# Optimization experiments

Measured on AMD Instinct MI355X. Metric: run time of the kernel, lower is better.

The kernel has to match this reference:

```python
import jax, jax.numpy as jnp
import numpy as np

N_NODES = 50000
N_EDGES = 600000
D_IN = 128
D_HID = 128


def _graph_conv(x, src, dst, W, b, n_nodes):
    # DGL GraphConv with norm='both': out = D_in^{-1/2} A (D_out^{-1/2} x) W + b
    ones = jnp.ones(src.shape[0], dtype=x.dtype)
    deg_out = jnp.maximum(jax.ops.segment_sum(ones, src, num_segments=n_nodes), 1.0)
    deg_in = jnp.maximum(jax.ops.segment_sum(ones, dst, num_segments=n_nodes), 1.0)
    h = x * (deg_out ** -0.5)[:, None]            # [N, d] scale by src-side norm
    agg = jax.ops.segment_sum(h[src], dst, num_segments=n_nodes)  # SpMM aggregate
    agg = agg * (deg_in ** -0.5)[:, None]
    return agg @ W + b


def _two_layer(x, src, dst, W1, b1, W2, b2):
    h = jax.nn.relu(_graph_conv(x, src, dst, W1, b1, N_NODES))
    return jax.nn.relu(_graph_conv(h, src, dst, W2, b2, N_NODES))


def setup_inputs() -> dict:
    key = jax.random.key(0)
    ks = jax.random.split(key, 16)
    inp = {}
    for i in range(4):
        inp[f"x{i+1}"] = jax.random.normal(ks[3 * i], (N_NODES, D_IN), dtype=jnp.float32)
        inp[f"src{i+1}"] = jax.random.randint(ks[3 * i + 1], (N_EDGES,), 0, N_NODES)
        inp[f"dst{i+1}"] = jax.random.randint(ks[3 * i + 2], (N_EDGES,), 0, N_NODES)
    inp["W1"] = jax.random.normal(ks[12], (D_IN, D_HID), dtype=jnp.float32) * (D_IN ** -0.5)
    inp["b1"] = jnp.zeros((D_HID,), dtype=jnp.float32)
    inp["W2"] = jax.random.normal(ks[13], (D_HID, D_HID), dtype=jnp.float32) * (D_HID ** -0.5)
    inp["b2"] = jnp.zeros((D_HID,), dtype=jnp.float32)
    return inp


def reference(x1, src1, dst1, x2, src2, dst2, x3, src3, dst3, x4, src4, dst4,
              W1, b1, W2, b2):
    h1 = _two_layer(x1, src1, dst1, W1, b1, W2, b2)
    h2 = _two_layer(x2, src2, dst2, W1, b1, W2, b2)
    h3 = _two_layer(x3, src3, dst3, W1, b1, W2, b2)
    h4 = _two_layer(x4, src4, dst4, W1, b1, W2, b2)
    # multi_graph_opt='mean': concat along node axis, mean over nodes -> [D_HID]
    x = jnp.mean(jnp.concatenate([h1, h2, h3, h4], axis=0), axis=0)
    # output_opt='mean': scalar
    return jnp.mean(x)
```

## Files before the change

kernel.cpp:

```cpp
#include <hip/hip_runtime.h>
#include <hip/hip_bf16.h>

#define N_NODES 50000
#define N_EDGES 600000
#define D 128

#define NBUCK 64
#define BUCK_R 782
#define BCAP 16384
#define EPB 2048

typedef __attribute__((ext_vector_type(8))) short bf16x8;
typedef __attribute__((ext_vector_type(4))) float f32x4;
typedef __attribute__((ext_vector_type(2))) float f32x2;

__device__ __forceinline__ const int* pick4(const int* a, const int* b,
                                            const int* c, const int* d, int g) {
    return g == 0 ? a : g == 1 ? b : g == 2 ? c : d;
}
__device__ __forceinline__ const float4* pick4f(const float4* a, const float4* b,
                                                const float4* c, const float4* d, int g) {
    return g == 0 ? a : g == 1 ? b : g == 2 ? c : d;
}

__device__ __forceinline__ unsigned bfpair(float a, float b) {
    unsigned ua = __float_as_uint(a); ua = (ua + 0x7FFF + ((ua >> 16) & 1)) >> 16;
    unsigned ub = __float_as_uint(b); ub = (ub + 0x7FFF + ((ub >> 16) & 1)) >> 16;
    return ua | (ub << 16);
}

__global__ __launch_bounds__(256) void phaseA_kernel(
        const int* s0, const int* s1, const int* s2, const int* s3,
        const int* d0, const int* d1, const int* d2, const int* d3,
        int* __restrict__ bCurD, int* __restrict__ bCurS,
        int* __restrict__ pairs, unsigned short* __restrict__ svals, int nEdges) {
    int gi = blockIdx.y;
    const int* src = pick4(s0, s1, s2, s3, gi);
    const int* dst = pick4(d0, d1, d2, d3, gi);
    int* pg = pairs + (size_t)gi * NBUCK * BCAP;
    unsigned short* sg = svals + (size_t)gi * NBUCK * BCAP;

    __shared__ int cntD[64], cntS[64], gposD[64], gposS[64], lcurD[64], lcurS[64];
    int t = threadIdx.x;
    if (t < 64) { cntD[t] = 0; cntS[t] = 0; }
    __syncthreads();

    int myD[8], myS[8];
    int base = blockIdx.x * EPB + t;
    #pragma unroll
    for (int j = 0; j < 8; ++j) {
        int e = base + j * 256;
        if (e < nEdges) {
            myD[j] = dst[e]; myS[j] = src[e];
            atomicAdd(&cntD[myD[j] / BUCK_R], 1);
            atomicAdd(&cntS[myS[j] / BUCK_R], 1);
        } else myD[j] = -1;
    }
    __syncthreads();
    if (t < 64) {
        int c = cntD[t];
        gposD[t] = t * BCAP + (c ? atomicAdd(&bCurD[gi * 64 + t], c) : 0);
        lcurD[t] = 0;
        c = cntS[t];
        gposS[t] = t * BCAP + (c ? atomicAdd(&bCurS[gi * 64 + t], c) : 0);
        lcurS[t] = 0;
    }
    __syncthreads();
    #pragma unroll
    for (int j = 0; j < 8; ++j) {
        if (myD[j] >= 0) {
            int bD = myD[j] / BUCK_R, bS = myS[j] / BUCK_R;
            int lp = atomicAdd(&lcurD[bD], 1);
            pg[gposD[bD] + lp] = ((myD[j] - bD * BUCK_R) << 16) | myS[j];
            int ls = atomicAdd(&lcurS[bS], 1);
            sg[gposS[bS] + ls] = (unsigned short)(myS[j] - bS * BUCK_R);
        }
    }
}

__global__ __launch_bounds__(256) void csrB_kernel(
        const int* __restrict__ bCurD, const int* __restrict__ pairs,
        int* __restrict__ rowptrBase, int* __restrict__ eixBase,
        float* __restrict__ rsIBase) {
    int gi = blockIdx.y, b = blockIdx.x;
    int* rowptr = rowptrBase + (size_t)gi * (N_NODES + 1);
    int* eidx = eixBase + (size_t)gi * N_EDGES;
    float* rsI = rsIBase + (size_t)gi * N_NODES;
    const int* pg = pairs + ((size_t)gi * NBUCK + b) * BCAP;
    const int* bCur = bCurD + gi * 64;

    __shared__ int P[BCAP];
    __shared__ int cnt[1024];
    __shared__ int cur[1024];
    __shared__ int wpart[4];
    __shared__ int sbase;

    int t = threadIdx.x;
    int nb = bCur[b]; if (nb > BCAP) nb = BCAP;

    if (t < 64) {
        int v = (t < b) ? min(bCur[t], BCAP) : 0;
        for (int off = 32; off; off >>= 1) v += __shfl_down(v, off, 64);
        if (t == 0) sbase = v;
    }
    for (int i = t; i < 1024; i += 256) cnt[i] = 0;
    __syncthreads();
    int base = sbase;

    for (int i = t; i < nb; i += 256) {
        int p = pg[i];
        P[i] = p;
        atomicAdd(&cnt[p >> 16], 1);
    }
    __syncthreads();

    int c0 = cnt[t * 4 + 0], c1 = cnt[t * 4 + 1], c2 = cnt[t * 4 + 2], c3 = cnt[t * 4 + 3];
    int ts = c0 + c1 + c2 + c3;
    int lane = t & 63, w = t >> 6;
    int incl = ts;
    for (int off = 1; off < 64; off <<= 1) {
        int u = __shfl_up(incl, off, 64);
        if (lane >= off) incl += u;
    }
    if (lane == 63) wpart[w] = incl;
    __syncthreads();
    int wb = 0;
    #pragma unroll
    for (int i = 0; i < 4; ++i) if (i < w) wb += wpart[i];
    int ex = wb + incl - ts;
    cur[t * 4 + 0] = ex;
    cur[t * 4 + 1] = ex + c0;
    cur[t * 4 + 2] = ex + c0 + c1;
    cur[t * 4 + 3] = ex + c0 + c1 + c2;
    __syncthreads();

    int lo = b * BUCK_R;
    int nh = N_NODES - lo; if (nh > BUCK_R) nh = BUCK_R;
    for (int i = t; i < nh; i += 256) {
        rowptr[lo + i] = base + cur[i];
        rsI[lo + i] = 1.0f / sqrtf(fmaxf((float)cnt[i], 1.0f));
    }
    if (b == NBUCK - 1 && t == 0) rowptr[N_NODES] = N_EDGES;
    __syncthreads();

    for (int i = t; i < nb; i += 256) {
        int p = P[i];
        int pos = atomicAdd(&cur[p >> 16], 1);
        eidx[base + pos] = p & 0xFFFF;
    }
}

__global__ __launch_bounds__(256) void csrC_kernel(
        const int* __restrict__ bCurS, const unsigned short* __restrict__ svals,
        float* __restrict__ rsOBase) {
    int gi = blockIdx.y, b = blockIdx.x;
    float* rsO = rsOBase + (size_t)gi * N_NODES;
    const unsigned short* sg = svals + ((size_t)gi * NBUCK + b) * BCAP;
    __shared__ int cnt[1024];
    int t = threadIdx.x;
    for (int i = t; i < 1024; i += 256) cnt[i] = 0;
    __syncthreads();
    int ns = bCurS[gi * 64 + b]; if (ns > BCAP) ns = BCAP;
    for (int i = t; i < ns; i += 256) atomicAdd(&cnt[sg[i]], 1);
    __syncthreads();
    int lo = b * BUCK_R;
    int nh = N_NODES - lo; if (nh > BUCK_R) nh = BUCK_R;
    for (int i = t; i < nh; i += 256)
        rsO[lo + i] = 1.0f / sqrtf(fmaxf((float)cnt[i], 1.0f));
}

__global__ void wconv_kernel(const float* __restrict__ W1, const float* __restrict__ W2,
                             unsigned* __restrict__ Wp1, unsigned* __restrict__ Wp2) {
    const float* W = blockIdx.y ? W2 : W1;
    unsigned* Wp = blockIdx.y ? Wp2 : Wp1;
    int o = blockIdx.x * 256 + threadIdx.x;
    int j2 = o & 3, lane = (o >> 2) & 63, nt = (o >> 8) & 7, kc = o >> 11;
    int k = kc * 32 + (lane >> 4) * 8 + j2 * 2;
    int col = nt * 16 + (lane & 15);
    Wp[o] = bfpair(W[k * 128 + col], W[(k + 1) * 128 + col]);
}

__global__ void xconv_kernel(const float4* x0, const float4* x1,
                             const float4* x2, const float4* x3,
                             const float* __restrict__ rsOBase,
                             uint2* __restrict__ xbBase, int gFirst, int n ) {
    int gi = blockIdx.y;
    const float4* x = pick4f(x0, x1, x2, x3, gFirst + gi);
    const float* rsO = rsOBase + (size_t)(gFirst + gi) * N_NODES;
    uint2* xb = xbBase + (size_t)gi * (N_NODES * 16);
    int i = blockIdx.x * blockDim.x + threadIdx.x;
    if (i >= n) return;
    float sc = rsO[i >> 4];
    float4 a = x[i * 2];
    float4 b = x[i * 2 + 1];
    int w0 = __builtin_amdgcn_cvt_pk_fp8_f32(a.x * sc, a.y * sc, 0, false);
    w0 = __builtin_amdgcn_cvt_pk_fp8_f32(a.z * sc, a.w * sc, w0, true);
    int w1 = __builtin_amdgcn_cvt_pk_fp8_f32(b.x * sc, b.y * sc, 0, false);
    w1 = __builtin_amdgcn_cvt_pk_fp8_f32(b.z * sc, b.w * sc, w1, true);
    xb[i] = make_uint2((unsigned)w0, (unsigned)w1);
}

#define NCH32 1563

#define ACC16(U)                                                            \
    {                                                                       \
        f32x2 e0 = __builtin_amdgcn_cvt_pk_f32_fp8((U).x, false);           \
        f32x2 e1 = __builtin_amdgcn_cvt_pk_f32_fp8((U).x, true);            \
        f32x2 e2 = __builtin_amdgcn_cvt_pk_f32_fp8((U).y, false);           \
        f32x2 e3 = __builtin_amdgcn_cvt_pk_f32_fp8((U).y, true);            \
        f32x2 e4 = __builtin_amdgcn_cvt_pk_f32_fp8((U).z, false);           \
        f32x2 e5 = __builtin_amdgcn_cvt_pk_f32_fp8((U).z, true);            \
        f32x2 e6 = __builtin_amdgcn_cvt_pk_f32_fp8((U).w, false);           \
        f32x2 e7 = __builtin_amdgcn_cvt_pk_f32_fp8((U).w, true);            \
        a[0] += e0[0];  a[1] += e0[1];  a[2] += e1[0];  a[3] += e1[1];      \
        a[4] += e2[0];  a[5] += e2[1];  a[6] += e3[0];  a[7] += e3[1];      \
        a[8] += e4[0];  a[9] += e4[1];  a[10] += e5[0]; a[11] += e5[1];     \
        a[12] += e6[0]; a[13] += e6[1]; a[14] += e7[0]; a[15] += e7[1];     \
    }

template <int LAYER>
__global__ __launch_bounds__(256) void fused_kernel(
        const int* __restrict__ rowptrBase, const int* __restrict__ eixBase,
        const unsigned char* __restrict__ hBase,
        const float* __restrict__ rsIBase, const float* __restrict__ rsOBase,
        const uint4* __restrict__ Wp, const float* __restrict__ bias,
        unsigned char* __restrict__ outBase, double* __restrict__ acc, int gFirst) {
    const int gi = blockIdx.y;
    const int g = gFirst + gi;
    const int* rowptr = rowptrBase + (size_t)g * (N_NODES + 1);
    const int* eidx   = eixBase + (size_t)g * N_EDGES;
    const float* rsI  = rsIBase + (size_t)g * N_NODES;
    const float* rsO  = rsOBase + (size_t)g * N_NODES;
    const unsigned char* h = hBase + (size_t)gi * N_NODES * D;
    unsigned char* outb = outBase + (size_t)gi * N_NODES * D;

    __shared__ unsigned short A[32][136];

    const int t = threadIdx.x;
    const int row = t >> 3;
    const int sub = t & 7;
    const int lane = t & 63, wv = t >> 6;
    const int l15 = lane & 15, lh = lane >> 4;

    bf16x8 bfr[4][2];
    #pragma unroll
    for (int kc = 0; kc < 4; ++kc)
        #pragma unroll
        for (int j = 0; j < 2; ++j) {
            uint4 u = Wp[(kc * 8 + wv * 2 + j) * 64 + lane];
            bfr[kc][j] = *(bf16x8*)&u;
        }
    float bv[2];
    #pragma unroll
    for (int j = 0; j < 2; ++j) bv[j] = bias[wv * 32 + j * 16 + l15];

    const int ch = blockIdx.x;
    const int r = ch * 32 + row;
    int p = 0, pend = 0;
    float sc = 0.f;
    if (r < N_NODES) { p = rowptr[r]; pend = rowptr[r + 1]; sc = rsI[r]; }

    float a[16];
    #pragma unroll
    for (int j = 0; j < 16; ++j) a[j] = 0.f;
    const unsigned char* hp = h + sub * 16;
    for (; p + 4 <= pend; p += 4) {
        uint4 u0 = *(const uint4*)(hp + (size_t)eidx[p] * 128);
        uint4 u1 = *(const uint4*)(hp + (size_t)eidx[p + 1] * 128);
        uint4 u2 = *(const uint4*)(hp + (size_t)eidx[p + 2] * 128);
        uint4 u3 = *(const uint4*)(hp + (size_t)eidx[p + 3] * 128);
        ACC16(u0) ACC16(u1) ACC16(u2) ACC16(u3)
    }
    for (; p < pend; ++p) {
        uint4 u0 = *(const uint4*)(hp + (size_t)eidx[p] * 128);
        ACC16(u0)
    }
    {
        uint4 pkA, pkB;
        pkA.x = bfpair(a[0] * sc, a[1] * sc);
        pkA.y = bfpair(a[2] * sc, a[3] * sc);
        pkA.z = bfpair(a[4] * sc, a[5] * sc);
        pkA.w = bfpair(a[6] * sc, a[7] * sc);
        pkB.x = bfpair(a[8] * sc, a[9] * sc);
        pkB.y = bfpair(a[10] * sc, a[11] * sc);
        pkB.z = bfpair(a[12] * sc, a[13] * sc);
        pkB.w = bfpair(a[14] * sc, a[15] * sc);
        *(uint4*)&A[row][sub * 16]     = pkA;
        *(uint4*)&A[row][sub * 16 + 8] = pkB;
    }
    __syncthreads();

    f32x4 c[2][2];
    #pragma unroll
    for (int ti = 0; ti < 2; ++ti) {
        c[ti][0] = (f32x4){0.f, 0.f, 0.f, 0.f};
        c[ti][1] = (f32x4){0.f, 0.f, 0.f, 0.f};
    }
    #pragma unroll
    for (int ti = 0; ti < 2; ++ti) {
        #pragma unroll
        for (int kc = 0; kc < 4; ++kc) {
            uint4 u = *(const uint4*)&A[ti * 16 + l15][kc * 32 + lh * 8];
            bf16x8 afr = *(bf16x8*)&u;
            c[ti][0] = __builtin_amdgcn_mfma_f32_16x16x32_bf16(afr, bfr[kc][0], c[ti][0], 0, 0, 0);
            c[ti][1] = __builtin_amdgcn_mfma_f32_16x16x32_bf16(afr, bfr[kc][1], c[ti][1], 0, 0, 0);
        }
    }

    double lsum = 0.0;
    #pragma unroll
    for (int ti = 0; ti < 2; ++ti) {
        const int r0 = ch * 32 + ti * 16 + lh * 4;
        #pragma unroll
        for (int jj = 0; jj < 4; ++jj) {
            int rr = r0 + jj;
            if (rr < N_NODES) {
                float o0 = fmaxf(c[ti][0][jj] + bv[0], 0.f);
                float o1 = fmaxf(c[ti][1][jj] + bv[1], 0.f);
                if (LAYER == 2) {
                    lsum += (double)o0 + (double)o1;
                } else {
                    float s2 = rsO[rr];
                    float q0 = o0 * s2, q1 = o1 * s2;
                    unsigned b0 = (unsigned)__builtin_amdgcn_cvt_pk_fp8_f32(q0, q0, 0, false);
                    unsigned b1 = (unsigned)__builtin_amdgcn_cvt_pk_fp8_f32(q1, q1, 0, false);
                    outb[(size_t)rr * 128 + wv * 32 + l15]      = (unsigned char)(b0 & 0xFF);
                    outb[(size_t)rr * 128 + wv * 32 + 16 + l15] = (unsigned char)(b1 & 0xFF);
                }
            }
        }
    }

    if (LAYER == 2) {
        for (int off = 32; off; off >>= 1) lsum += __shfl_down(lsum, off, 64);
        __shared__ double wred[4];
        if (lane == 0) wred[wv] = lsum;
        __syncthreads();
        if (t == 0) atomicAdd(acc, wred[0] + wred[1] + wred[2] + wred[3]);
    }
}

__global__ void finalize_kernel(const double* __restrict__ acc, float* __restrict__ out) {
    if (threadIdx.x == 0 && blockIdx.x == 0)
        out[0] = (float)(acc[0] / (4.0 * N_NODES * D));
}

extern "C" void kernel_launch(void* const* d_in, const int* in_sizes, int n_in,
                              void* d_out, int out_size, void* d_ws, size_t ws_size,
                              hipStream_t stream) {
    const float* x[4];
    const int* src[4];
    const int* dst[4];
    for (int g = 0; g < 4; ++g) {
        x[g]   = (const float*)d_in[3 * g + 0];
        src[g] = (const int*)  d_in[3 * g + 1];
        dst[g] = (const int*)  d_in[3 * g + 2];
    }
    const float* W1 = (const float*)d_in[12];
    const float* b1 = (const float*)d_in[13];
    const float* W2 = (const float*)d_in[14];
    const float* b2 = (const float*)d_in[15];
    float* out = (float*)d_out;

    int* ws32 = (int*)d_ws;
    double* acc     = (double*)d_ws;
    int* bCurD      = ws32 + 64;
    int* bCurS      = ws32 + 320;
    unsigned* Wp1   = (unsigned*)(ws32 + 1024);
    unsigned* Wp2   = Wp1 + 8192;
    int* rowptrBase = ws32 + 17408;
    float* rsIBase  = (float*)(ws32 + 217412);
    float* rsOBase  = (float*)(ws32 + 417412);
    int* eixBase    = ws32 + 617412;
    int* pairs      = ws32 + 3017412;
    unsigned short* svals = (unsigned short*)(pairs + 4194304);
    unsigned char* xbA    = (unsigned char*)(ws32 + 3017412);

    auto needBytes = [](int gb) -> size_t {
        size_t ov = (size_t)gb * 3200000;
        if (ov < 6291456) ov = 6291456;
        return (3017412 + ov) * 4;
    };
    int gb = 1;
    if (ws_size >= needBytes(4)) gb = 4;
    else if (ws_size >= needBytes(2)) gb = 2;
    unsigned char* AbA = xbA + (size_t)gb * N_NODES * D;

    const int paGrid    = (N_EDGES + EPB - 1) / EPB;
    const int xconvGrid = (N_NODES * 16 + 255) / 256;

    hipMemsetAsync(d_ws, 0, 1024 * sizeof(int), stream);

    wconv_kernel<<<dim3(32, 2), 256, 0, stream>>>(W1, W2, Wp1, Wp2);
    phaseA_kernel<<<dim3(paGrid, 4), 256, 0, stream>>>(
        src[0], src[1], src[2], src[3], dst[0], dst[1], dst[2], dst[3],
        bCurD, bCurS, pairs, svals, N_EDGES);
    csrB_kernel<<<dim3(NBUCK, 4), 256, 0, stream>>>(
        bCurD, pairs, rowptrBase, eixBase, rsIBase);
    csrC_kernel<<<dim3(NBUCK, 4), 256, 0, stream>>>(bCurS, svals, rsOBase);

    for (int g0 = 0; g0 < 4; g0 += gb) {
        int nb = 4 - g0 < gb ? 4 - g0 : gb;
        xconv_kernel<<<dim3(xconvGrid, nb), 256, 0, stream>>>(
            (const float4*)x[0], (const float4*)x[1], (const float4*)x[2], (const float4*)x[3],
            rsOBase, (uint2*)xbA, g0, N_NODES * 16);
        fused_kernel<1><<<dim3(NCH32, nb), 256, 0, stream>>>(
            rowptrBase, eixBase, xbA, rsIBase, rsOBase,
            (const uint4*)Wp1, b1, AbA, nullptr, g0);
        fused_kernel<2><<<dim3(NCH32, nb), 256, 0, stream>>>(
            rowptrBase, eixBase, AbA, rsIBase, rsOBase,
            (const uint4*)Wp2, b2, nullptr, acc, g0);
    }

    finalize_kernel<<<1, 64, 0, stream>>>(acc, out);
}
```

Baseline: 280.7 us.

## Sort each row's neighbor indices into source-node slabs for gather locality

```diff
diff --git a/kernel.cpp b/kernel.cpp
--- a/kernel.cpp
+++ b/kernel.cpp
@@ -9,6 +9,9 @@
 #define BUCK_R 782
 #define BCAP 16384
 #define EPB 2048
+
+#define SL_SHIFT 13
+#define NSL 8
 
 typedef __attribute__((ext_vector_type(8))) short bf16x8;
 typedef __attribute__((ext_vector_type(4))) float f32x4;
@@ -167,6 +170,36 @@
     int nh = N_NODES - lo; if (nh > BUCK_R) nh = BUCK_R;
     for (int i = t; i < nh; i += 256)
         rsO[lo + i] = 1.0f / sqrtf(fmaxf((float)cnt[i], 1.0f));
+}
+
+__global__ __launch_bounds__(256) void rowsort_kernel(
+        const int* __restrict__ rowptrBase, const int* __restrict__ eixBase,
+        int* __restrict__ rp8Base, int* __restrict__ eix2Base) {
+    int gi = blockIdx.y;
+    int r = blockIdx.x * 256 + threadIdx.x;
+    if (r >= N_NODES) return;
+    const int* rowptr = rowptrBase + (size_t)gi * (N_NODES + 1);
+    const int* eidx   = eixBase + (size_t)gi * N_EDGES;
+    int* rp8   = rp8Base + (size_t)gi * N_NODES * NSL;
+    int* eidx2 = eix2Base + (size_t)gi * N_EDGES;
+
+    int beg = rowptr[r], end = rowptr[r + 1];
+    unsigned long long cnt = 0ULL;
+    for (int p = beg; p < end; ++p)
+        cnt += 1ULL << ((unsigned)(eidx[p] >> SL_SHIFT) * 8);
+    unsigned long long incl = cnt;
+    incl += incl << 8; incl += incl << 16; incl += incl << 32;
+    unsigned long long excl = incl << 8;
+    #pragma unroll
+    for (int s = 0; s < NSL; ++s)
+        rp8[(size_t)r * NSL + s] = beg + (int)((excl >> (s * 8)) & 0xFF);
+    unsigned long long cur = excl;
+    for (int p = beg; p < end; ++p) {
+        int v = eidx[p];
+        unsigned s8 = (unsigned)(v >> SL_SHIFT) * 8;
+        eidx2[beg + (int)((cur >> s8) & 0xFF)] = v;
+        cur += 1ULL << s8;
+    }
 }
 
 __global__ void wconv_kernel(const float* __restrict__ W1, const float* __restrict__ W2,
@@ -220,7 +253,8 @@
 
 template <int LAYER>
 __global__ __launch_bounds__(256) void fused_kernel(
-        const int* __restrict__ rowptrBase, const int* __restrict__ eixBase,
+        const int* __restrict__ rowptrBase, const int* __restrict__ rp8Base,
+        const int* __restrict__ eix2Base,
         const unsigned char* __restrict__ hBase,
         const float* __restrict__ rsIBase, const float* __restrict__ rsOBase,
         const uint4* __restrict__ Wp, const float* __restrict__ bias,
@@ -228,7 +262,8 @@
     const int gi = blockIdx.y;
     const int g = gFirst + gi;
     const int* rowptr = rowptrBase + (size_t)g * (N_NODES + 1);
-    const int* eidx   = eixBase + (size_t)g * N_EDGES;
+    const int* rp8    = rp8Base + (size_t)g * N_NODES * NSL;
+    const int* eidx   = eix2Base + (size_t)g * N_EDGES;
     const float* rsI  = rsIBase + (size_t)g * N_NODES;
     const float* rsO  = rsOBase + (size_t)g * N_NODES;
     const unsigned char* h = hBase + (size_t)gi * N_NODES * D;
@@ -256,24 +291,34 @@
 
     const int ch = blockIdx.x;
     const int r = ch * 32 + row;
-    int p = 0, pend = 0;
     float sc = 0.f;
-    if (r < N_NODES) { p = rowptr[r]; pend = rowptr[r + 1]; sc = rsI[r]; }
+    int rp[NSL + 1];
+    if (r < N_NODES) {
+        #pragma unroll
+        for (int s = 0; s < NSL; ++s) rp[s] = rp8[(size_t)r * NSL + s];
+        rp[NSL] = rowptr[r + 1];
+        sc = rsI[r];
+    } else {
+        #pragma unroll
+        for (int s = 0; s <= NSL; ++s) rp[s] = 0;
+    }
 
     float a[16];
     #pragma unroll
     for (int j = 0; j < 16; ++j) a[j] = 0.f;
     const unsigned char* hp = h + sub * 16;
-    for (; p + 4 <= pend; p += 4) {
-        uint4 u0 = *(const uint4*)(hp + (size_t)eidx[p] * 128);
-        uint4 u1 = *(const uint4*)(hp + (size_t)eidx[p + 1] * 128);
-        uint4 u2 = *(const uint4*)(hp + (size_t)eidx[p + 2] * 128);
-        uint4 u3 = *(const uint4*)(hp + (size_t)eidx[p + 3] * 128);
-        ACC16(u0) ACC16(u1) ACC16(u2) ACC16(u3)
-    }
-    for (; p < pend; ++p) {
-        uint4 u0 = *(const uint4*)(hp + (size_t)eidx[p] * 128);
-        ACC16(u0)
+    #pragma unroll
+    for (int s = 0; s < NSL; ++s) {
+        int p = rp[s], pe = rp[s + 1];
+        for (; p + 2 <= pe; p += 2) {
+            uint4 u0 = *(const uint4*)(hp + (size_t)eidx[p] * 128);
+            uint4 u1 = *(const uint4*)(hp + (size_t)eidx[p + 1] * 128);
+            ACC16(u0) ACC16(u1)
+        }
+        if (p < pe) {
+            uint4 u0 = *(const uint4*)(hp + (size_t)eidx[p] * 128);
+            ACC16(u0)
+        }
     }
     {
         uint4 pkA, pkB;
@@ -376,18 +421,24 @@
     unsigned short* svals = (unsigned short*)(pairs + 4194304);
     unsigned char* xbA    = (unsigned char*)(ws32 + 3017412);
 
-    auto needBytes = [](int gb) -> size_t {
+    auto overlayUnits = [](int gb) -> size_t {
         size_t ov = (size_t)gb * 3200000;
         if (ov < 6291456) ov = 6291456;
-        return (3017412 + ov) * 4;
+        return ov;
+    };
+    auto needBytes = [&](int gb) -> size_t {
+        return (3017412 + overlayUnits(gb) + 1600000 + 2400000) * 4 + 4096;
     };
     int gb = 1;
     if (ws_size >= needBytes(4)) gb = 4;
     else if (ws_size >= needBytes(2)) gb = 2;
     unsigned char* AbA = xbA + (size_t)gb * N_NODES * D;
+    int* rp8Base  = ws32 + 3017412 + overlayUnits(gb);
+    int* eix2Base = rp8Base + 1600000;
 
     const int paGrid    = (N_EDGES + EPB - 1) / EPB;
     const int xconvGrid = (N_NODES * 16 + 255) / 256;
+    const int sortGrid  = (N_NODES + 255) / 256;
 
     hipMemsetAsync(d_ws, 0, 1024 * sizeof(int), stream);
 
@@ -398,6 +449,8 @@
     csrB_kernel<<<dim3(NBUCK, 4), 256, 0, stream>>>(
         bCurD, pairs, rowptrBase, eixBase, rsIBase);
     csrC_kernel<<<dim3(NBUCK, 4), 256, 0, stream>>>(bCurS, svals, rsOBase);
+    rowsort_kernel<<<dim3(sortGrid, 4), 256, 0, stream>>>(
+        rowptrBase, eixBase, rp8Base, eix2Base);
 
     for (int g0 = 0; g0 < 4; g0 += gb) {
         int nb = 4 - g0 < gb ? 4 - g0 : gb;
@@ -405,10 +458,10 @@
             (const float4*)x[0], (const float4*)x[1], (const float4*)x[2], (const float4*)x[3],
             rsOBase, (uint2*)xbA, g0, N_NODES * 16);
         fused_kernel<1><<<dim3(NCH32, nb), 256, 0, stream>>>(
-            rowptrBase, eixBase, xbA, rsIBase, rsOBase,
+            rowptrBase, rp8Base, eix2Base, xbA, rsIBase, rsOBase,
             (const uint4*)Wp1, b1, AbA, nullptr, g0);
         fused_kernel<2><<<dim3(NCH32, nb), 256, 0, stream>>>(
-            rowptrBase, eixBase, AbA, rsIBase, rsOBase,
+            rowptrBase, rp8Base, eix2Base, AbA, rsIBase, rsOBase,
             (const uint4*)Wp2, b2, nullptr, acc, g0);
     }
 
```

After: 364.3 us. 1.3x slower.
